# Optimization experiments

Hardware: AMD Instinct MI355X
Metric: run time of the kernel (lower is better)

The kernel has to match this reference:

```python
import jax, jax.numpy as jnp
import numpy as np

NUM_HEADS = 16
ATTN_WINDOW = 128  # half-width; mask is |i-j| <= ATTN_WINDOW
EMBED_DIM = 1024


def setup_inputs() -> dict:
    key = jax.random.key(0)
    ks = jax.random.split(key, 9)
    B, S, D = 2, 2048, EMBED_DIM
    s = 1.0 / np.sqrt(D)
    inp = {
        "x": jax.random.normal(ks[0], (B, S, D), dtype=jnp.float32),
        "Wq": jax.random.normal(ks[1], (D, D), dtype=jnp.float32) * s,
        "bq": jnp.zeros((D,), dtype=jnp.float32),
        "Wk": jax.random.normal(ks[2], (D, D), dtype=jnp.float32) * s,
        "bk": jnp.zeros((D,), dtype=jnp.float32),
        "Wv": jax.random.normal(ks[3], (D, D), dtype=jnp.float32) * s,
        "bv": jnp.zeros((D,), dtype=jnp.float32),
        "Wo": jax.random.normal(ks[4], (D, D), dtype=jnp.float32) * s,
        "bo": jnp.zeros((D,), dtype=jnp.float32),
    }
    return inp


def reference(x, Wq, bq, Wk, bk, Wv, bv, Wo, bo):
    B, S, D = x.shape
    H = NUM_HEADS
    dh = D // H
    # projections (nn.Linear: x @ W^T + b)
    q = (x @ Wq.T + bq).reshape(B, S, H, dh).transpose(0, 2, 1, 3)  # [B,H,S,dh]
    k = (x @ Wk.T + bk).reshape(B, S, H, dh).transpose(0, 2, 1, 3)
    v = (x @ Wv.T + bv).reshape(B, S, H, dh).transpose(0, 2, 1, 3)
    scale = 1.0 / jnp.sqrt(jnp.asarray(dh, dtype=jnp.float32))
    scores = jnp.einsum("bhqd,bhkd->bhqk", q, k) * scale  # [B,H,S,S]
    # sliding-window band mask: allowed iff |i - j| <= ATTN_WINDOW
    idx = jnp.arange(S)
    band = jnp.abs(idx[:, None] - idx[None, :]) <= ATTN_WINDOW  # [S,S] bool
    scores = jnp.where(band[None, None], scores, -jnp.inf)
    attn = jax.nn.softmax(scores, axis=-1)  # each row has >=1 valid entry
    ctx = jnp.einsum("bhqk,bhkd->bhqd", attn, v)
    ctx = ctx.transpose(0, 2, 1, 3).reshape(B, S, D)
    out = ctx @ Wo.T + bo
    return out, attn
```

## Files before the change

kernel.cpp:

```cpp
#include <hip/hip_runtime.h>
#include <cstddef>

#define NB 2
#define NH 16
#define SQ 2048
#define DM 1024
#define DH 64
#define WN 128

using half8  = __attribute__((ext_vector_type(8))) _Float16;
using half4  = __attribute__((ext_vector_type(4))) _Float16;
using floatx4 = __attribute__((ext_vector_type(4))) float;

__device__ __forceinline__ void gl_lds16(const _Float16* g, _Float16* l) {
    __builtin_amdgcn_global_load_lds(
        (const __attribute__((address_space(1))) void*)g,
        (__attribute__((address_space(3))) void*)l, 16, 0, 0);
}

__global__ __launch_bounds__(256) void cvt1(const float* __restrict__ s,
                                            _Float16* __restrict__ d, int n8)
{
    int idx = blockIdx.x * 256 + threadIdx.x;
    if (idx < n8) {
        const float4 a = ((const float4*)s)[idx * 2];
        const float4 b = ((const float4*)s)[idx * 2 + 1];
        half8 h;
        h[0] = (_Float16)a.x; h[1] = (_Float16)a.y;
        h[2] = (_Float16)a.z; h[3] = (_Float16)a.w;
        h[4] = (_Float16)b.x; h[5] = (_Float16)b.y;
        h[6] = (_Float16)b.z; h[7] = (_Float16)b.w;
        ((half8*)d)[idx] = h;
    }
}

__global__ __launch_bounds__(256) void cvt4(
    const float* __restrict__ s0, const float* __restrict__ s1,
    const float* __restrict__ s2, const float* __restrict__ s3,
    _Float16* __restrict__ d0, _Float16* __restrict__ d1,
    _Float16* __restrict__ d2, _Float16* __restrict__ d3, int n8)
{
    const float* s = (blockIdx.y == 0) ? s0 : (blockIdx.y == 1) ? s1
                   : (blockIdx.y == 2) ? s2 : s3;
    _Float16*   d = (blockIdx.y == 0) ? d0 : (blockIdx.y == 1) ? d1
                   : (blockIdx.y == 2) ? d2 : d3;
    int idx = blockIdx.x * 256 + threadIdx.x;
    if (idx < n8) {
        const float4 a = ((const float4*)s)[idx * 2];
        const float4 b = ((const float4*)s)[idx * 2 + 1];
        half8 h;
        h[0] = (_Float16)a.x; h[1] = (_Float16)a.y;
        h[2] = (_Float16)a.z; h[3] = (_Float16)a.w;
        h[4] = (_Float16)b.x; h[5] = (_Float16)b.y;
        h[6] = (_Float16)b.z; h[7] = (_Float16)b.w;
        ((half8*)d)[idx] = h;
    }
}

template <int OUT_HALF>
__global__ __launch_bounds__(256) void gemm_h(
    const _Float16* __restrict__ A,
    const _Float16* __restrict__ W0, const _Float16* __restrict__ W1,
    const _Float16* __restrict__ W2,
    const float* __restrict__ b0, const float* __restrict__ b1,
    const float* __restrict__ b2,
    void* __restrict__ O0, void* __restrict__ O1, void* __restrict__ O2)
{
    constexpr int K = DM, N = DM, BK = 64;

    const _Float16* Wp = (blockIdx.z == 0) ? W0 : (blockIdx.z == 1) ? W1 : W2;
    const float*    bb = (blockIdx.z == 0) ? b0 : (blockIdx.z == 1) ? b1 : b2;
    void*           Op = (blockIdx.z == 0) ? O0 : (blockIdx.z == 1) ? O1 : O2;

    __shared__ _Float16 Asl[128 * BK];
    __shared__ _Float16 Bsl[128 * BK];

    const int tid  = threadIdx.x;
    const int lane = tid & 63;
    const int w    = tid >> 6;
    const int wm   = w & 1, wn = w >> 1;
    const int m0   = blockIdx.y * 128;
    const int n0   = blockIdx.x * 128;

    const int l8 = lane >> 3;
    const int lc = lane & 7;

    floatx4 acc[4][4];
#pragma unroll
    for (int t = 0; t < 4; ++t)
#pragma unroll
        for (int u = 0; u < 4; ++u) acc[t][u] = (floatx4){0.f, 0.f, 0.f, 0.f};

    for (int k0 = 0; k0 < K; k0 += BK) {
        __syncthreads();
#pragma unroll
        for (int i = 0; i < 4; ++i) {
            const int r  = w * 8 + l8 + i * 32;
            const int ca = lc ^ (r & 7);
            gl_lds16(A  + (size_t)(m0 + r) * K + k0 + ca * 8,
                     Asl + r * BK + lc * 8);
            gl_lds16(Wp + (size_t)(n0 + r) * K + k0 + ca * 8,
                     Bsl + r * BK + lc * 8);
        }
        __syncthreads();
#pragma unroll
        for (int kk = 0; kk < BK; kk += 32) {
            half8 af[4], bf[4];
            const int q = (kk >> 3) + (lane >> 4);
#pragma unroll
            for (int t = 0; t < 4; ++t) {
                const int ra = wm * 64 + t * 16 + (lane & 15);
                af[t] = *(const half8*)(Asl + ra * BK + ((q ^ (ra & 7)) << 3));
                const int rb = wn * 64 + t * 16 + (lane & 15);
                bf[t] = *(const half8*)(Bsl + rb * BK + ((q ^ (rb & 7)) << 3));
            }
#pragma unroll
            for (int t = 0; t < 4; ++t)
#pragma unroll
                for (int u = 0; u < 4; ++u)
                    acc[t][u] = __builtin_amdgcn_mfma_f32_16x16x32_f16(
                        af[t], bf[u], acc[t][u], 0, 0, 0);
        }
    }

    const int col0 = n0 + wn * 64 + (lane & 15);
    const int row0 = m0 + wm * 64 + ((lane >> 4) << 2);
#pragma unroll
    for (int u = 0; u < 4; ++u) {
        const int n = col0 + u * 16;
        const float bias = bb[n];
#pragma unroll
        for (int t = 0; t < 4; ++t) {
            const int m = row0 + t * 16;
#pragma unroll
            for (int r = 0; r < 4; ++r) {
                const float v = acc[t][u][r] + bias;
                if (OUT_HALF)
                    ((_Float16*)Op)[(size_t)(m + r) * N + n] = (_Float16)v;
                else
                    ((float*)Op)[(size_t)(m + r) * N + n] = v;
            }
        }
    }
}

__global__ __launch_bounds__(256) void attn_mfma(
    const _Float16* __restrict__ Q, const _Float16* __restrict__ K,
    const _Float16* __restrict__ V, float* __restrict__ attn,
    _Float16* __restrict__ ctx)
{
    const int tid  = threadIdx.x;
    const int lane = tid & 63;
    const int w    = tid >> 6;
    const int h = blockIdx.y, b = blockIdx.z;
    const int i0 = blockIdx.x * 16;
    const int wo = i0 - WN;

    __shared__ _Float16 KV[64 * 320];
    __shared__ _Float16 Qs[16 * 64];
    __shared__ float    Sl[16 * 276];
    __shared__ _Float16 Pl[16 * 320];

    const int l8 = lane >> 3;
    const int lc = lane & 7;

#pragma unroll
    for (int i = 0; i < 8; ++i) {
        const int r  = w * 8 + l8 + i * 32;
        const int jg = wo + r;
        const int jc = jg < 0 ? 0 : (jg >= SQ ? SQ - 1 : jg);
        const int ca = lc ^ (r & 7);
        gl_lds16(K + ((size_t)(b * SQ + jc)) * DM + h * DH + ca * 8,
                 KV + r * 64 + lc * 8);
    }
    if (w < 2) {
        const int r  = 256 + w * 8 + l8;
        const int jg = wo + r;
        const int jc = jg >= SQ ? SQ - 1 : jg;
        const int ca = lc ^ (r & 7);
        gl_lds16(K + ((size_t)(b * SQ + jc)) * DM + h * DH + ca * 8,
                 KV + r * 64 + lc * 8);
    } else {
        const int r  = (w - 2) * 8 + l8;
        const int ca = lc ^ (r & 7);
        gl_lds16(Q + ((size_t)(b * SQ + i0 + r)) * DM + h * DH + ca * 8,
                 Qs + r * 64 + lc * 8);
    }

    half8 vr[9];
#pragma unroll
    for (int it = 0; it < 9; ++it) {
        const int idx = tid + 256 * it;
        const int j = idx >> 3, c8 = idx & 7;
        const int jg = wo + j;
        const int jc = jg < 0 ? 0 : (jg >= SQ ? SQ - 1 : jg);
        vr[it] = *(const half8*)(V + ((size_t)(b * SQ + jc)) * DM + h * DH + c8 * 8);
    }

    __syncthreads();

    half8 af0, af1;
    {
        const int row = lane & 15;
        af0 = *(const half8*)(Qs + row * 64 + ((((lane >> 4))     ^ (row & 7)) << 3));
        af1 = *(const half8*)(Qs + row * 64 + (((4 + (lane >> 4)) ^ (row & 7)) << 3));
    }
    for (int t = w; t < 17; t += 4) {
        const int rb = t * 16 + (lane & 15);
        half8 bf0 = *(const half8*)(KV + rb * 64 + ((((lane >> 4))     ^ (rb & 7)) << 3));
        half8 bf1 = *(const half8*)(KV + rb * 64 + (((4 + (lane >> 4)) ^ (rb & 7)) << 3));
        floatx4 acc = (floatx4){0.f, 0.f, 0.f, 0.f};
        acc = __builtin_amdgcn_mfma_f32_16x16x32_f16(af0, bf0, acc, 0, 0, 0);
        acc = __builtin_amdgcn_mfma_f32_16x16x32_f16(af1, bf1, acc, 0, 0, 0);
        const int jloc = t * 16 + (lane & 15);
        const int jg   = wo + jloc;
        const bool inr = (jg >= 0) && (jg < SQ);
#pragma unroll
        for (int r = 0; r < 4; ++r) {
            const int q = ((lane >> 4) << 2) + r;
            const bool valid = ((unsigned)(jloc - q) <= 256u) && inr;
            Sl[q * 276 + jloc] = valid ? acc[r] * 0.125f : -1e30f;
        }
    }
    __syncthreads();

#pragma unroll
    for (int it = 0; it < 9; ++it) {
        const int idx = tid + 256 * it;
        const int j = idx >> 3, c8 = idx & 7;
        const int jc3 = j >> 3, jl = j & 7;
#pragma unroll
        for (int e = 0; e < 8; ++e) {
            const int d = c8 * 8 + e;
            KV[d * 320 + ((jc3 ^ ((c8 + e) & 7)) << 3) + jl] = vr[it][e];
        }
    }

    for (int q = w; q < 16; q += 4) {
        const float* Srow = Sl + q * 276;
        const float v0 = Srow[lane];
        const float v1 = Srow[lane + 64];
        const float v2 = Srow[lane + 128];
        const float v3 = Srow[lane + 192];
        const float v4 = (lane < 16) ? Srow[lane + 256] : -1e30f;
        float m = fmaxf(fmaxf(fmaxf(v0, v1), fmaxf(v2, v3)), v4);
        m = fmaxf(m, __shfl_xor(m, 32));
        m = fmaxf(m, __shfl_xor(m, 16));
        m = fmaxf(m, __shfl_xor(m, 8));
        m = fmaxf(m, __shfl_xor(m, 4));
        m = fmaxf(m, __shfl_xor(m, 2));
        m = fmaxf(m, __shfl_xor(m, 1));
        float e0 = __expf(v0 - m), e1 = __expf(v1 - m), e2 = __expf(v2 - m),
              e3 = __expf(v3 - m), e4 = __expf(v4 - m);
        float s = ((e0 + e1) + (e2 + e3)) + e4;
        s += __shfl_xor(s, 32); s += __shfl_xor(s, 16); s += __shfl_xor(s, 8);
        s += __shfl_xor(s, 4);  s += __shfl_xor(s, 2);  s += __shfl_xor(s, 1);
        const float inv = 1.0f / s;
        e0 *= inv; e1 *= inv; e2 *= inv; e3 *= inv; e4 *= inv;

        const int fq = (q + (q >> 3)) & 7;
        _Float16* Prow = Pl + q * 320;
        Prow[((((lane      ) >> 3) ^ fq) << 3) + (lane & 7)] = (_Float16)e0;
        Prow[((((lane +  64) >> 3) ^ fq) << 3) + (lane & 7)] = (_Float16)e1;
        Prow[((((lane + 128) >> 3) ^ fq) << 3) + (lane & 7)] = (_Float16)e2;
        Prow[((((lane + 192) >> 3) ^ fq) << 3) + (lane & 7)] = (_Float16)e3;
        if (lane < 16) {
            Prow[((((lane + 256) >> 3) ^ fq) << 3) + (lane & 7)] = (_Float16)e4;
            Prow[((((lane + 272) >> 3) ^ fq) << 3) + (lane & 7)] = (_Float16)0.f;
        }

        float* arow = attn + ((size_t)(b * NH + h) * SQ + i0 + q) * SQ;
        const int g0 = wo + lane;
        if ((unsigned)(g0      ) < (unsigned)SQ) arow[g0      ] = e0;
        if ((unsigned)(g0 +  64) < (unsigned)SQ) arow[g0 +  64] = e1;
        if ((unsigned)(g0 + 128) < (unsigned)SQ) arow[g0 + 128] = e2;
        if ((unsigned)(g0 + 192) < (unsigned)SQ) arow[g0 + 192] = e3;
        if (lane < 16 && (unsigned)(g0 + 256) < (unsigned)SQ) arow[g0 + 256] = e4;
        const int a0 = wo > 0 ? wo : 0;
        const int b0 = (wo + 272 < SQ) ? (wo + 272) : SQ;
        const float4 z4 = make_float4(0.f, 0.f, 0.f, 0.f);
        float4* za = (float4*)arow;
        const int na = a0 >> 2;
        for (int c = lane; c < na; c += 64) za[c] = z4;
        float4* zb = (float4*)(arow + b0);
        const int nb = (SQ - b0) >> 2;
        for (int c = lane; c < nb; c += 64) zb[c] = z4;
    }
    __syncthreads();

    {
        const int rowp = lane & 15;
        const int fp = (rowp + (rowp >> 3)) & 7;
        const int rowv = w * 16 + (lane & 15);
        const int fv = (rowv + (rowv >> 3)) & 7;
        floatx4 acc = (floatx4){0.f, 0.f, 0.f, 0.f};
#pragma unroll
        for (int ks = 0; ks < 9; ++ks) {
            const int lch = ks * 4 + (lane >> 4);
            half8 ap = *(const half8*)(Pl + rowp * 320 + ((lch ^ fp) << 3));
            half8 bp = *(const half8*)(KV + rowv * 320 + ((lch ^ fv) << 3));
            acc = __builtin_amdgcn_mfma_f32_16x16x32_f16(ap, bp, acc, 0, 0, 0);
        }
        const int dcol = w * 16 + (lane & 15);
#pragma unroll
        for (int r = 0; r < 4; ++r) {
            const int q = ((lane >> 4) << 2) + r;
            ctx[((size_t)(b * SQ + i0 + q)) * DM + h * DH + dcol] = (_Float16)acc[r];
        }
    }
}

extern "C" void kernel_launch(void* const* d_in, const int* in_sizes, int n_in,
                              void* d_out, int out_size, void* d_ws, size_t ws_size,
                              hipStream_t stream)
{
    const float* x  = (const float*)d_in[0];
    const float* Wq = (const float*)d_in[1];
    const float* bq = (const float*)d_in[2];
    const float* Wk = (const float*)d_in[3];
    const float* bk = (const float*)d_in[4];
    const float* Wv = (const float*)d_in[5];
    const float* bv = (const float*)d_in[6];
    const float* Wo = (const float*)d_in[7];
    const float* bo = (const float*)d_in[8];

    float* out  = (float*)d_out;
    float* attn = out + (size_t)NB * SQ * DM;

    const size_t tok = (size_t)NB * SQ * DM;
    const size_t wsz = (size_t)DM * DM;

    _Float16* xh   = (_Float16*)d_ws;
    _Float16* Wqh  = xh   + tok;
    _Float16* Wkh  = Wqh  + wsz;
    _Float16* Wvh  = Wkh  + wsz;
    _Float16* Woh  = Wvh  + wsz;
    _Float16* Qh   = Woh  + wsz;
    _Float16* Kh   = Qh   + tok;
    _Float16* Vh   = Kh   + tok;
    _Float16* ctxh = Vh   + tok;

    cvt1<<<dim3((int)(tok / 8 / 256)), dim3(256), 0, stream>>>(x, xh, (int)(tok / 8));
    cvt4<<<dim3((int)(wsz / 8 / 256), 4), dim3(256), 0, stream>>>(
        Wq, Wk, Wv, Wo, Wqh, Wkh, Wvh, Woh, (int)(wsz / 8));

    gemm_h<1><<<dim3(DM / 128, (NB * SQ) / 128, 3), dim3(256), 0, stream>>>(
        xh, Wqh, Wkh, Wvh, bq, bk, bv, Qh, Kh, Vh);

    attn_mfma<<<dim3(SQ / 16, NH, NB), dim3(256), 0, stream>>>(Qh, Kh, Vh, attn, ctxh);

    gemm_h<0><<<dim3(DM / 128, (NB * SQ) / 128, 1), dim3(256), 0, stream>>>(
        ctxh, Woh, Woh, Woh, bo, bo, bo, out, out, out);
}
```

Baseline: 660.9 us.

## Shrink attention LDS footprint and hoist attn zero-fill ahead of the first barrier

The separate score and probability LDS buffers become one shared byte buffer, where each wave writes its fp16 probability row over the float score row it has already read into registers. The V-transpose row stride drops from 320 to 288 halves, with a 2-bit swizzle to match. Total LDS falls enough to request three blocks per CU via launch_bounds, where the old layout allowed about two. The zero-fill of the out-of-band attn entries moves before the first barrier and is spread across all threads, so those stores overlap with the K/Q/V loads. The aliasing relies on the in-wave read-before-write ordering, and the narrower swizzle may increase LDS bank conflicts.

```diff
diff --git a/kernel.cpp b/kernel.cpp
--- a/kernel.cpp
+++ b/kernel.cpp
@@ -144,7 +144,7 @@
     }
 }
 
-__global__ __launch_bounds__(256) void attn_mfma(
+__global__ __launch_bounds__(256, 3) void attn_mfma(
     const _Float16* __restrict__ Q, const _Float16* __restrict__ K,
     const _Float16* __restrict__ V, float* __restrict__ attn,
     _Float16* __restrict__ ctx)
@@ -156,10 +156,10 @@
     const int i0 = blockIdx.x * 16;
     const int wo = i0 - WN;
 
-    __shared__ _Float16 KV[64 * 320];
-    __shared__ _Float16 Qs[16 * 64];
-    __shared__ float    Sl[16 * 276];
-    __shared__ _Float16 Pl[16 * 320];
+    __shared__ __align__(16) char smem[54272];
+    _Float16* KV = (_Float16*)smem;
+    _Float16* Qs = (_Float16*)(smem + 34816);
+    char*     Sb = smem + 36864;
 
     const int l8 = lane >> 3;
     const int lc = lane & 7;
@@ -197,6 +197,19 @@
         vr[it] = *(const half8*)(V + ((size_t)(b * SQ + jc)) * DM + h * DH + c8 * 8);
     }
 
+    {
+        const int a0 = wo > 0 ? wo : 0;
+        const int b0 = (wo + 272 < SQ) ? (wo + 272) : SQ;
+        const float4 z4 = make_float4(0.f, 0.f, 0.f, 0.f);
+        float* abase = attn + ((size_t)(b * NH + h) * SQ + i0) * SQ;
+        for (int idx = tid; idx < 16 * 512; idx += 256) {
+            const int r  = idx >> 9;
+            const int c4 = (idx & 511) << 2;
+            if (c4 < a0 || c4 >= b0)
+                *(float4*)(abase + (size_t)r * SQ + c4) = z4;
+        }
+    }
+
     __syncthreads();
 
     half8 af0, af1;
@@ -219,7 +232,7 @@
         for (int r = 0; r < 4; ++r) {
             const int q = ((lane >> 4) << 2) + r;
             const bool valid = ((unsigned)(jloc - q) <= 256u) && inr;
-            Sl[q * 276 + jloc] = valid ? acc[r] * 0.125f : -1e30f;
+            ((float*)(Sb + q * 1088))[jloc] = valid ? acc[r] * 0.125f : -1e30f;
         }
     }
     __syncthreads();
@@ -231,13 +244,14 @@
         const int jc3 = j >> 3, jl = j & 7;
 #pragma unroll
         for (int e = 0; e < 8; ++e) {
-            const int d = c8 * 8 + e;
-            KV[d * 320 + ((jc3 ^ ((c8 + e) & 7)) << 3) + jl] = vr[it][e];
+            const int d  = c8 * 8 + e;
+            const int f2 = (d + (d >> 3)) & 3;
+            KV[d * 288 + ((jc3 ^ f2) << 3) + jl] = vr[it][e];
         }
     }
 
     for (int q = w; q < 16; q += 4) {
-        const float* Srow = Sl + q * 276;
+        const float* Srow = (const float*)(Sb + q * 1088);
         const float v0 = Srow[lane];
         const float v1 = Srow[lane + 64];
         const float v2 = Srow[lane + 128];
@@ -259,14 +273,15 @@
         e0 *= inv; e1 *= inv; e2 *= inv; e3 *= inv; e4 *= inv;
 
         const int fq = (q + (q >> 3)) & 7;
-        _Float16* Prow = Pl + q * 320;
+        _Float16* Prow = (_Float16*)(Sb + q * 1088);
         Prow[((((lane      ) >> 3) ^ fq) << 3) + (lane & 7)] = (_Float16)e0;
         Prow[((((lane +  64) >> 3) ^ fq) << 3) + (lane & 7)] = (_Float16)e1;
         Prow[((((lane + 128) >> 3) ^ fq) << 3) + (lane & 7)] = (_Float16)e2;
         Prow[((((lane + 192) >> 3) ^ fq) << 3) + (lane & 7)] = (_Float16)e3;
         if (lane < 16) {
             Prow[((((lane + 256) >> 3) ^ fq) << 3) + (lane & 7)] = (_Float16)e4;
-            Prow[((((lane + 272) >> 3) ^ fq) << 3) + (lane & 7)] = (_Float16)0.f;
+            Prow[((((lane + 272) >> 3) ^ fq) << 3) + (lane & 7)] =
+                (_Float16)(0.0f * e4);
         }
 
         float* arow = attn + ((size_t)(b * NH + h) * SQ + i0 + q) * SQ;
@@ -276,15 +291,6 @@
         if ((unsigned)(g0 + 128) < (unsigned)SQ) arow[g0 + 128] = e2;
         if ((unsigned)(g0 + 192) < (unsigned)SQ) arow[g0 + 192] = e3;
         if (lane < 16 && (unsigned)(g0 + 256) < (unsigned)SQ) arow[g0 + 256] = e4;
-        const int a0 = wo > 0 ? wo : 0;
-        const int b0 = (wo + 272 < SQ) ? (wo + 272) : SQ;
-        const float4 z4 = make_float4(0.f, 0.f, 0.f, 0.f);
-        float4* za = (float4*)arow;
-        const int na = a0 >> 2;
-        for (int c = lane; c < na; c += 64) za[c] = z4;
-        float4* zb = (float4*)(arow + b0);
-        const int nb = (SQ - b0) >> 2;
-        for (int c = lane; c < nb; c += 64) zb[c] = z4;
     }
     __syncthreads();
 
@@ -292,13 +298,13 @@
         const int rowp = lane & 15;
         const int fp = (rowp + (rowp >> 3)) & 7;
         const int rowv = w * 16 + (lane & 15);
-        const int fv = (rowv + (rowv >> 3)) & 7;
+        const int fv = (rowv + (rowv >> 3)) & 3;
         floatx4 acc = (floatx4){0.f, 0.f, 0.f, 0.f};
 #pragma unroll
         for (int ks = 0; ks < 9; ++ks) {
             const int lch = ks * 4 + (lane >> 4);
-            half8 ap = *(const half8*)(Pl + rowp * 320 + ((lch ^ fp) << 3));
-            half8 bp = *(const half8*)(KV + rowv * 320 + ((lch ^ fv) << 3));
+            half8 ap = *(const half8*)(Sb + rowp * 1088 + ((lch ^ fp) << 4));
+            half8 bp = *(const half8*)(KV + rowv * 288 + ((lch ^ fv) << 3));
             acc = __builtin_amdgcn_mfma_f32_16x16x32_f16(ap, bp, acc, 0, 0, 0);
         }
         const int dcol = w * 16 + (lane & 15);
```

After: 666.4 us. No clear change (+0.8%).
